# Optimization experiments

Hardware: AMD Instinct MI355X
Metric: run time of the kernel (lower is better)

Reference implementation:

```python
import jax, jax.numpy as jnp
import numpy as np

FEAT_STRIDE = 16
SCALES = (4, 8, 16, 32)
RATIOS = (0.5, 1.0, 2.0)
A = len(SCALES) * len(RATIOS)  # 12 anchors per location
PRE_NMS = 6000
POST_NMS = 300
NMS_THRESH = 0.7
MIN_SIZE = 16.0
B, C_IN, HF, WF = 4, 768, 64, 64


def _generate_anchors():
    base = np.array([0.0, 0.0, 15.0, 15.0])

    def whctrs(a):
        w = a[2] - a[0] + 1.0
        h = a[3] - a[1] + 1.0
        return w, h, a[0] + 0.5 * (w - 1.0), a[1] + 0.5 * (h - 1.0)

    def mk(ws, hs, xc, yc):
        ws = np.asarray(ws, dtype=np.float64)[:, None]
        hs = np.asarray(hs, dtype=np.float64)[:, None]
        return np.hstack([xc - 0.5 * (ws - 1), yc - 0.5 * (hs - 1),
                          xc + 0.5 * (ws - 1), yc + 0.5 * (hs - 1)])

    w, h, xc, yc = whctrs(base)
    size = w * h
    ratios = np.array(RATIOS)
    ws = np.round(np.sqrt(size / ratios))
    hs = np.round(ws * ratios)
    ratio_anchors = mk(ws, hs, xc, yc)
    scales = np.array(SCALES, dtype=np.float64)
    out = []
    for i in range(ratio_anchors.shape[0]):
        w, h, xc, yc = whctrs(ratio_anchors[i])
        out.append(mk(w * scales, h * scales, xc, yc))
    return np.vstack(out).astype(np.float32)  # (A, 4)


def _all_anchors(hf, wf):
    an = _generate_anchors()
    sx = np.arange(wf) * FEAT_STRIDE
    sy = np.arange(hf) * FEAT_STRIDE
    sx, sy = np.meshgrid(sx, sy)
    shifts = np.stack([sx.ravel(), sy.ravel(), sx.ravel(), sy.ravel()], axis=1).astype(np.float32)
    # shift-major, anchor-minor: (K, A, 4) -> (K*A, 4) matches bbox_pred layout
    return jnp.asarray((shifts[:, None, :] + an[None, :, :]).reshape(-1, 4))


def _conv(x, w, b):
    y = jax.lax.conv_general_dilated(x, w, (1, 1), 'SAME',
                                     dimension_numbers=('NCHW', 'OIHW', 'NCHW'))
    return y + b[None, :, None, None]


def _decode(anchors, deltas):
    w = anchors[:, 2] - anchors[:, 0] + 1.0
    h = anchors[:, 3] - anchors[:, 1] + 1.0
    cx = anchors[:, 0] + 0.5 * w
    cy = anchors[:, 1] + 0.5 * h
    dx, dy, dw, dh = deltas[:, 0], deltas[:, 1], deltas[:, 2], deltas[:, 3]
    pcx = dx * w + cx
    pcy = dy * h + cy
    pw = jnp.exp(dw) * w
    ph = jnp.exp(dh) * h
    return jnp.stack([pcx - 0.5 * pw, pcy - 0.5 * ph,
                      pcx + 0.5 * pw, pcy + 0.5 * ph], axis=1)


def _nms_keep(boxes, thresh):
    # greedy NMS on score-sorted boxes; returns boolean keep mask
    boxes = jax.lax.stop_gradient(boxes)
    n = boxes.shape[0]
    x1, y1, x2, y2 = boxes[:, 0], boxes[:, 1], boxes[:, 2], boxes[:, 3]
    areas = (x2 - x1 + 1.0) * (y2 - y1 + 1.0)
    idx = jnp.arange(n)

    def body(keep, i):
        xx1 = jnp.maximum(x1[i], x1)
        yy1 = jnp.maximum(y1[i], y1)
        xx2 = jnp.minimum(x2[i], x2)
        yy2 = jnp.minimum(y2[i], y2)
        inter = jnp.maximum(xx2 - xx1 + 1.0, 0.0) * jnp.maximum(yy2 - yy1 + 1.0, 0.0)
        iou = inter / (areas[i] + areas - inter)
        suppress = (iou > thresh) & (idx > i) & keep[i]
        return keep & ~suppress, None

    keep, _ = jax.lax.scan(body, jnp.ones(n, dtype=bool), jnp.arange(n))
    return keep


def _proposal_single(scores, deltas, anchors, im_info):
    # scores: (N,), deltas: (N,4), im_info: (3,) = [h, w, scale]
    boxes = _decode(anchors, deltas)
    x1 = jnp.clip(boxes[:, 0], 0.0, im_info[1] - 1.0)
    y1 = jnp.clip(boxes[:, 1], 0.0, im_info[0] - 1.0)
    x2 = jnp.clip(boxes[:, 2], 0.0, im_info[1] - 1.0)
    y2 = jnp.clip(boxes[:, 3], 0.0, im_info[0] - 1.0)
    boxes = jnp.stack([x1, y1, x2, y2], axis=1)
    ms = MIN_SIZE * im_info[2]
    valid = ((x2 - x1 + 1.0) >= ms) & ((y2 - y1 + 1.0) >= ms)
    scores = jnp.where(valid, scores, -jnp.inf)
    _, top_idx = jax.lax.top_k(scores, PRE_NMS)
    boxes = boxes[top_idx]
    keep = _nms_keep(boxes, NMS_THRESH)
    # first POST_NMS kept indices (boxes already score-sorted); zero-pad shortfall
    sel = jnp.sort(jnp.where(keep, jnp.arange(PRE_NMS), PRE_NMS))[:POST_NMS]
    pad = sel == PRE_NMS
    sel = jnp.minimum(sel, PRE_NMS - 1)
    return boxes[sel] * (~pad)[:, None].astype(boxes.dtype)


def setup_inputs() -> dict:
    key = jax.random.key(0)
    ks = jax.random.split(key, 4)
    features = jax.random.normal(ks[0], (B, C_IN, HF, WF), dtype=jnp.float32)
    im_info = jnp.tile(jnp.array([[1024.0, 1024.0, 1.0]], dtype=jnp.float32), (B, 1))
    W1 = jax.random.normal(ks[1], (512, C_IN, 3, 3), dtype=jnp.float32) * (2.0 / (C_IN * 9)) ** 0.5
    b1 = jnp.zeros((512,), dtype=jnp.float32)
    Ws = jax.random.normal(ks[2], (2 * A, 512, 1, 1), dtype=jnp.float32) * 0.01
    bs = jnp.zeros((2 * A,), dtype=jnp.float32)
    Wb = jax.random.normal(ks[3], (4 * A, 512, 1, 1), dtype=jnp.float32) * 0.01
    bb = jnp.zeros((4 * A,), dtype=jnp.float32)
    return {"features": features, "im_info": im_info, "W1": W1, "b1": b1,
            "Ws": Ws, "bs": bs, "Wb": Wb, "bb": bb}


def reference(features, im_info, W1, b1, Ws, bs, Wb, bb):
    # RPN head: 3x3 conv + relu, then 1x1 score/bbox heads
    x = jax.nn.relu(_conv(features, W1, b1))
    cls = _conv(x, Ws, bs)       # (B, 2A, H, W)
    bbox = _conv(x, Wb, bb)      # (B, 4A, H, W)
    b, _, hf, wf = cls.shape
    # view(B, 2, -1, W) softmax over class dim, view back -> channels [0:A]=bg, [A:2A]=fg
    prob = jax.nn.softmax(cls.reshape(b, 2, -1, wf), axis=1).reshape(cls.shape)
    fg = prob[:, A:, :, :]
    scores = fg.transpose(0, 2, 3, 1).reshape(b, -1)          # (B, H*W*A)
    deltas = bbox.transpose(0, 2, 3, 1).reshape(b, -1, 4)     # (B, H*W*A, 4)
    anchors = _all_anchors(hf, wf)
    boxes = jax.vmap(lambda s, d, ii: _proposal_single(s, d, anchors, ii))(scores, deltas, im_info)
    batch_idx = jnp.repeat(jnp.arange(b, dtype=boxes.dtype), POST_NMS)[:, None]
    rois = jnp.concatenate([batch_idx, boxes.reshape(-1, 4)], axis=1)  # (B*POST_NMS, 5)
    return rois
```

## Files before the change

### kernel.cpp

```cpp
#include <hip/hip_runtime.h>
#include <stdint.h>

#define CIN 768
#define CMID 512
#define NPIX 4096
#define NANCH 49152
#define NBATCH 4
#define PRE_NMS_N 6000
#define POST_NMS_N 300

__global__ void zeroK(uint32_t* __restrict__ p, int nWords){
  int i = blockIdx.x * 256 + threadIdx.x;
  if (i < nWords) p[i] = 0u;
}

__global__ __launch_bounds__(256) void conv3x3K(
    const float* __restrict__ feat, const float* __restrict__ W1,
    const float* __restrict__ b1, float* __restrict__ xout){
  __shared__ float wLds[9920];
  __shared__ float fLds[960];
  const int tid = threadIdx.x;
  const int g  = tid >> 3;
  const int py = tid & 7;
  const int ty0 = (blockIdx.x >> 3) << 3;
  const int tx0 = (blockIdx.x & 7) << 3;
  const int ocb = blockIdx.y << 7;
  const int b = blockIdx.z;

  const int oc_t  = tid >> 1;
  const int halfw = tid & 1;
  const float* wsrc0 = W1 + (size_t)(ocb + oc_t)*6912 + halfw*36;
  const int gq   = (oc_t>>2)*12 + (oc_t&3)*3;
  const int icl0 = halfw << 2;

  int fdst[4]; int fsrc[4]; bool fgo[4]; bool fact[4];
#pragma unroll
  for (int i=0;i<4;i++){
    int lin = tid + (i<<8);
    fact[i] = lin < 800;
    int l2 = fact[i] ? lin : 0;
    int ic = l2/100; int r2 = l2 - ic*100;
    int row = r2/10; int col = r2 - row*10;
    int gy = ty0 + row - 1, gx = tx0 + col - 1;
    fgo[i]  = fact[i] && gy>=0 && gy<64 && gx>=0 && gx<64;
    fdst[i] = ic*120 + row*12 + col;
    fsrc[i] = (ic<<12) + (gy<<6) + gx;
  }
  const float* fbase = feat + ((size_t)(b*CIN) << 12);

  double macc[4][8];
  float cacc[4][8];
#pragma unroll
  for (int q=0;q<4;q++)
#pragma unroll
    for (int j=0;j<8;j++){ macc[q][j]=0.0; cacc[q][j]=0.0f; }

  for (int icb = 0; icb < CIN; icb += 8){
    {
      const float* s = wsrc0 + (size_t)icb*9;
      float w0[36];
#pragma unroll
      for (int m=0;m<9;m++){
        float4 v = *reinterpret_cast<const float4*>(s + (m<<2));
        w0[4*m+0]=v.x; w0[4*m+1]=v.y; w0[4*m+2]=v.z; w0[4*m+3]=v.w;
      }
#pragma unroll
      for (int r=0;r<4;r++)
#pragma unroll
        for (int k=0;k<9;k++)
          wLds[(icl0+r)*1152 + (k/3)*384 + gq + (k%3)] = w0[r*9+k];
    }
#pragma unroll
    for (int i=0;i<4;i++){
      if (fact[i]){
        float v = 0.0f;
        if (fgo[i]) v = fbase[((size_t)icb << 12) + fsrc[i]];
        fLds[fdst[i]] = v;
      }
    }
    __syncthreads();
#pragma unroll
    for (int ic=0; ic<8; ic++){
      const float* fb = &fLds[ic*120 + py*12];
      const float* wb = &wLds[ic*1152 + g*12];
#pragma unroll
      for (int ky=0;ky<3;ky++){
        float4 a = *reinterpret_cast<const float4*>(fb + ky*12);
        float4 c = *reinterpret_cast<const float4*>(fb + ky*12 + 4);
        float2 e = *reinterpret_cast<const float2*>(fb + ky*12 + 8);
        const float f[10] = {a.x,a.y,a.z,a.w,c.x,c.y,c.z,c.w,e.x,e.y};
        const float* wp = wb + ky*384;
        float4 wa = *reinterpret_cast<const float4*>(wp);
        float4 wv = *reinterpret_cast<const float4*>(wp+4);
        float4 wc = *reinterpret_cast<const float4*>(wp+8);
        const float w12[12] = {wa.x,wa.y,wa.z,wa.w, wv.x,wv.y,wv.z,wv.w,
                               wc.x,wc.y,wc.z,wc.w};
#pragma unroll
        for (int q=0;q<4;q++)
#pragma unroll
          for (int kx=0;kx<3;kx++){
            float we = w12[q*3+kx];
#pragma unroll
            for (int j=0;j<8;j++)
              cacc[q][j] = fmaf(we, f[j+kx], cacc[q][j]);
          }
      }
      if ((ic & 3) == 3){
#pragma unroll
        for (int q=0;q<4;q++)
#pragma unroll
          for (int j=0;j<8;j++){ macc[q][j] += (double)cacc[q][j]; cacc[q][j]=0.0f; }
      }
    }
    __syncthreads();
  }
#pragma unroll
  for (int q=0;q<4;q++){
    float bias = b1[ocb + (g<<2) + q];
    float4 o0, o1;
    float* p0 = (float*)&o0; float* p1 = (float*)&o1;
#pragma unroll
    for (int j=0;j<4;j++){
      p0[j] = fmaxf(__fadd_rn((float)macc[q][j],   bias), 0.0f);
      p1[j] = fmaxf(__fadd_rn((float)macc[q][j+4], bias), 0.0f);
    }
    size_t base = ((size_t)(b*CMID + ocb + (g<<2) + q) << 12) + ((ty0+py) << 6) + tx0;
    *reinterpret_cast<float4*>(&xout[base])     = o0;
    *reinterpret_cast<float4*>(&xout[base + 4]) = o1;
  }
}

__global__ __launch_bounds__(256) void conv1x1K(
    const float* __restrict__ x,
    const float* __restrict__ Ws, const float* __restrict__ bs,
    const float* __restrict__ Wb, const float* __restrict__ bb,
    float* __restrict__ clsRaw, float* __restrict__ bboxRaw){
  __shared__ float wLds[32*72];
  const int tid = threadIdx.x;
  const int px = tid & 63;
  const int og = tid >> 6;
  const int px0 = (blockIdx.x & 63) << 6;
  const int b = blockIdx.x >> 6;
  double m[18];
  float cc[18];
#pragma unroll
  for (int j=0;j<18;j++){ m[j]=0.0; cc[j]=0.0f; }
  for (int cb=0; cb<CMID; cb+=32){
#pragma unroll
    for (int i=0;i<9;i++){
      int lin = tid + i*256;
      int c = lin / 72;
      int j = lin - c*72;
      wLds[lin] = (j < 24) ? Ws[(size_t)j*512 + cb + c]
                           : Wb[(size_t)(j-24)*512 + cb + c];
    }
    __syncthreads();
    for (int c=0;c<32;c++){
      float xv = x[((size_t)(b*CMID + cb + c) << 12) + px0 + px];
      const float* wp = &wLds[c*72 + og*18];
#pragma unroll
      for (int j=0;j<18;j++) cc[j] = fmaf(wp[j], xv, cc[j]);
    }
#pragma unroll
    for (int j=0;j<18;j++){ m[j] += (double)cc[j]; cc[j]=0.0f; }
    __syncthreads();
  }
#pragma unroll
  for (int j=0;j<18;j++){
    int jg = og*18 + j;
    float bias = (jg < 24) ? bs[jg] : bb[jg-24];
    float v = __fadd_rn((float)m[j], bias);
    if (jg < 24) clsRaw[((size_t)(b*24 + jg) << 12) + px0 + px] = v;
    else         bboxRaw[((size_t)(b*48 + jg - 24) << 12) + px0 + px] = v;
  }
}

__global__ void decodeK(const float* __restrict__ clsRaw,
                        const float* __restrict__ bboxRaw,
                        const float* __restrict__ imInfo,
                        float* __restrict__ boxes, uint32_t* __restrict__ ubits,
                        uint32_t* __restrict__ hist1){
  int n = blockIdx.x*256 + threadIdx.x;
  if (n >= NBATCH*NANCH) return;
  int b = n / NANCH;
  int r = n - b*NANCH;
  int px = r / 12;
  int a = r - px*12;
  int yi = px >> 6, xi = px & 63;
  const int w0t[3] = {23,16,11};
  const int h0t[3] = {12,16,22};
  int ridx = a >> 2;
  int sh = 2 + (a & 3);
  float W = (float)(w0t[ridx] << sh);
  float H = (float)(h0t[ridx] << sh);
  float cx = (float)((xi << 4) + 8);
  float cy = (float)((yi << 4) + 8);

  size_t cbase = ((size_t)b*24 << 12) + px;
  float sc0 = clsRaw[cbase + ((size_t)a       << 12)];
  float sc1 = clsRaw[cbase + ((size_t)(12+a)  << 12)];
  size_t bbase = ((size_t)b*48 << 12) + px;
  float dx = bboxRaw[bbase + ((size_t)(4*a+0) << 12)];
  float dy = bboxRaw[bbase + ((size_t)(4*a+1) << 12)];
  float dw = bboxRaw[bbase + ((size_t)(4*a+2) << 12)];
  float dh = bboxRaw[bbase + ((size_t)(4*a+3) << 12)];

  float imh = imInfo[b*3+0], imw = imInfo[b*3+1], iscale = imInfo[b*3+2];

  float pcx = __fadd_rn(__fmul_rn(dx, W), cx);
  float pcy = __fadd_rn(__fmul_rn(dy, H), cy);
  float pw  = __fmul_rn(expf(dw), W);
  float ph  = __fmul_rn(expf(dh), H);
  float hw = __fmul_rn(0.5f, pw), hh = __fmul_rn(0.5f, ph);
  float x1 = __fsub_rn(pcx, hw), x2 = __fadd_rn(pcx, hw);
  float y1 = __fsub_rn(pcy, hh), y2 = __fadd_rn(pcy, hh);
  float xmax = __fsub_rn(imw, 1.0f), ymax = __fsub_rn(imh, 1.0f);
  x1 = fminf(fmaxf(x1, 0.0f), xmax);
  y1 = fminf(fmaxf(y1, 0.0f), ymax);
  x2 = fminf(fmaxf(x2, 0.0f), xmax);
  y2 = fminf(fmaxf(y2, 0.0f), ymax);
  float ms = __fmul_rn(16.0f, iscale);
  bool valid = (__fadd_rn(__fsub_rn(x2,x1),1.0f) >= ms) &&
               (__fadd_rn(__fsub_rn(y2,y1),1.0f) >= ms);

  float mm = fmaxf(sc0, sc1);
  float e0 = expf(__fsub_rn(sc0, mm));
  float e1 = expf(__fsub_rn(sc1, mm));
  float s  = __fdiv_rn(e1, __fadd_rn(e0, e1));

  uint32_t u = __float_as_uint(s);
  u = (u & 0x80000000u) ? ~u : (u | 0x80000000u);
  if (!valid) u = 0x007FFFFFu;

  float4 bx = make_float4(x1, y1, x2, y2);
  *reinterpret_cast<float4*>(&boxes[(size_t)n*4]) = bx;
  ubits[n] = u;
  atomicAdd(&hist1[((size_t)b << 16) + (u >> 16)], 1u);
}

__global__ void histLoK(const uint32_t* __restrict__ ubits,
                        const uint32_t* __restrict__ thrWS, uint32_t* __restrict__ hist2){
  int n = blockIdx.x*256 + threadIdx.x;
  if (n >= NBATCH*NANCH) return;
  int b = n / NANCH;
  uint32_t u = ubits[n];
  if ((u >> 16) == thrWS[b*4+0])
    atomicAdd(&hist2[((size_t)b << 16) + (u & 0xFFFFu)], 1u);
}

__global__ __launch_bounds__(1024) void selectK(const uint32_t* __restrict__ hist,
                                                uint32_t* __restrict__ thrWS, int stage){
  __shared__ uint32_t sA[1024];
  const int b = blockIdx.x;
  const uint32_t* h = hist + ((size_t)b << 16);
  const int tid = threadIdx.x;
  uint32_t base = (stage == 0) ? 0u : thrWS[b*4+1];
  uint32_t seg = 0;
  int b0 = tid << 6;
  for (int k=0;k<64;k++) seg += h[b0+k];
  sA[tid] = seg;
  __syncthreads();
  for (int off=1; off<1024; off<<=1){
    uint32_t v = (tid+off < 1024) ? sA[tid+off] : 0u;
    __syncthreads();
    sA[tid] += v;
    __syncthreads();
  }
  uint32_t inc = sA[tid];
  uint32_t above = inc - seg;
  if (base + above < 6000u && base + inc >= 6000u){
    uint32_t c = base + above;
    for (int bin = b0+63; bin >= b0; bin--){
      uint32_t hh = h[bin];
      if (c + hh >= 6000u){
        if (stage == 0){ thrWS[b*4+0] = (uint32_t)bin; thrWS[b*4+1] = c; }
        else { thrWS[b*4+2] = (thrWS[b*4+0] << 16) | (uint32_t)bin; thrWS[b*4+3] = c; }
        break;
      }
      c += hh;
    }
  }
}

__global__ void compactK(const uint32_t* __restrict__ ubits,
                         const uint32_t* __restrict__ thrWS,
                         uint32_t* __restrict__ cnts,
                         uint64_t* __restrict__ keyHi, uint64_t* __restrict__ keyEq){
  int n = blockIdx.x*256 + threadIdx.x;
  if (n >= NBATCH*NANCH) return;
  int b = n / NANCH;
  int r = n - b*NANCH;
  uint32_t u = ubits[n];
  uint32_t us = thrWS[b*4+2];
  if (u < us) return;
  uint64_t key = ((uint64_t)(~u) << 32) | (uint32_t)r;
  if (u > us){
    uint32_t p = atomicAdd(&cnts[b*2+0], 1u);
    if (p < 8192u) keyHi[((size_t)b << 13) + p] = key;
  } else {
    uint32_t p = atomicAdd(&cnts[b*2+1], 1u);
    if (p < 8192u) keyEq[((size_t)b << 13) + p] = key;
  }
}

__global__ __launch_bounds__(1024) void sortGatherK(
    const uint64_t* __restrict__ keyHi, const uint64_t* __restrict__ keyEq,
    const uint32_t* __restrict__ cnts, const float* __restrict__ boxes,
    float* __restrict__ rbox){
  __shared__ uint64_t keys[8192];
  const int b = blockIdx.x;
  const int tid = threadIdx.x;
  uint32_t nHi = cnts[b*2+0];
  if (nHi > 8192u) nHi = 8192u;
  uint32_t nEq = cnts[b*2+1];
  if (nEq > 8192u - nHi) nEq = 8192u - nHi;
  for (int i=tid; i<8192; i+=1024){
    uint64_t k;
    if (i < (int)nHi) k = keyHi[((size_t)b << 13) + i];
    else if (i < (int)(nHi + nEq)) k = keyEq[((size_t)b << 13) + (i - nHi)];
    else k = ~0ULL;
    keys[i] = k;
  }
  __syncthreads();
  for (unsigned kk = 2; kk <= 8192; kk <<= 1){
    for (unsigned j = kk >> 1; j > 0; j >>= 1){
      for (unsigned i = tid; i < 8192; i += 1024){
        unsigned l = i ^ j;
        if (l > i){
          bool up = ((i & kk) == 0);
          uint64_t a = keys[i], c = keys[l];
          if ((a > c) == up){ keys[i] = c; keys[l] = a; }
        }
      }
      __syncthreads();
    }
  }
  for (int r = tid; r < PRE_NMS_N; r += 1024){
    uint32_t idx = (uint32_t)(keys[r] & 0xFFFFFFFFu);
    float4 v = *reinterpret_cast<const float4*>(&boxes[((size_t)b*NANCH + idx)*4]);
    *reinterpret_cast<float4*>(&rbox[((size_t)b*PRE_NMS_N + r)*4]) = v;
  }
}

__global__ __launch_bounds__(64) void nmsMaskK(const float* __restrict__ rbox,
                                               uint64_t* __restrict__ mask){
  const int b = blockIdx.z;
  const int ib = blockIdx.y;
  const int jb = blockIdx.x;
  const int lane = threadIdx.x;
  uint64_t* mrow = &mask[(size_t)b*PRE_NMS_N*96];
  if (jb < ib){
    int ig = (ib << 6) + lane;
    if (ig < PRE_NMS_N) mrow[(size_t)ig*96 + jb] = 0ull;
    return;
  }
  __shared__ float rb[64][4];
  const int ig0 = ib << 6;
  {
    int ig = ig0 + lane;
    float4 v = make_float4(0.f,0.f,0.f,0.f);
    if (ig < PRE_NMS_N) v = *reinterpret_cast<const float4*>(&rbox[((size_t)b*PRE_NMS_N + ig)*4]);
    rb[lane][0]=v.x; rb[lane][1]=v.y; rb[lane][2]=v.z; rb[lane][3]=v.w;
  }
  const int jg = (jb << 6) + lane;
  const bool jok = jg < PRE_NMS_N;
  float4 cb = make_float4(0.f,0.f,0.f,0.f);
  if (jok) cb = *reinterpret_cast<const float4*>(&rbox[((size_t)b*PRE_NMS_N + jg)*4]);
  float areaJ = __fmul_rn(__fadd_rn(__fsub_rn(cb.z,cb.x),1.0f),
                          __fadd_rn(__fsub_rn(cb.w,cb.y),1.0f));
  __syncthreads();
#pragma unroll 4
  for (int i=0;i<64;i++){
    int ig = ig0 + i;
    if (ig >= PRE_NMS_N) break;
    float x1=rb[i][0], y1=rb[i][1], x2=rb[i][2], y2=rb[i][3];
    float areaI = __fmul_rn(__fadd_rn(__fsub_rn(x2,x1),1.0f),
                            __fadd_rn(__fsub_rn(y2,y1),1.0f));
    float xx1 = fmaxf(x1, cb.x);
    float yy1 = fmaxf(y1, cb.y);
    float xx2 = fminf(x2, cb.z);
    float yy2 = fminf(y2, cb.w);
    float ww = fmaxf(__fadd_rn(__fsub_rn(xx2,xx1),1.0f), 0.0f);
    float hh = fmaxf(__fadd_rn(__fsub_rn(yy2,yy1),1.0f), 0.0f);
    float inter = __fmul_rn(ww,hh);
    float iou = __fdiv_rn(inter, __fsub_rn(__fadd_rn(areaI, areaJ), inter));
    bool bit = jok && (jg > ig) && (iou > 0.7f);
    uint64_t wword = __ballot(bit);
    if (lane == 0) mrow[(size_t)ig*96 + jb] = wword;
  }
}

__global__ __launch_bounds__(64) void nmsScanK(const float* __restrict__ rbox,
                                               const uint64_t* __restrict__ mask,
                                               float* __restrict__ out){
  const int b = blockIdx.x;
  const int lane = threadIdx.x;
  const uint64_t* mrow = &mask[(size_t)b*PRE_NMS_N*96];
  uint64_t s0 = 0ull, s1 = 0ull;
  int cnt = 0;
  for (int i=0; i<PRE_NMS_N; i++){
    int w = i >> 6;
    uint64_t sw = (w < 64) ? __shfl(s0, w) : __shfl(s1, w-64);
    if (!((sw >> (i & 63)) & 1ull)){
      if (lane == 0){
        const float* s = &rbox[((size_t)b*PRE_NMS_N + i)*4];
        float* o = &out[(size_t)(b*POST_NMS_N + cnt)*5];
        o[0] = (float)b; o[1]=s[0]; o[2]=s[1]; o[3]=s[2]; o[4]=s[3];
      }
      cnt++;
      if (cnt == POST_NMS_N) break;
      const uint64_t* mr = mrow + (size_t)i*96;
      s0 |= mr[lane];
      if (lane < 30) s1 |= mr[64+lane];
    }
  }
  for (int r = cnt + lane; r < POST_NMS_N; r += 64){
    float* o = &out[(size_t)(b*POST_NMS_N + r)*5];
    o[0] = (float)b; o[1]=0.f; o[2]=0.f; o[3]=0.f; o[4]=0.f;
  }
}

extern "C" void kernel_launch(void* const* d_in, const int* in_sizes, int n_in,
                              void* d_out, int out_size, void* d_ws, size_t ws_size,
                              hipStream_t stream) {
  const float* features = (const float*)d_in[0];
  const float* im_info  = (const float*)d_in[1];
  const float* W1 = (const float*)d_in[2];
  const float* b1 = (const float*)d_in[3];
  const float* Ws = (const float*)d_in[4];
  const float* bs = (const float*)d_in[5];
  const float* Wb = (const float*)d_in[6];
  const float* bb = (const float*)d_in[7];
  float* out = (float*)d_out;
  char* ws = (char*)d_ws;

  const size_t offX     = 0;
  const size_t offCls   = offX     + (size_t)4*512*4096*4;
  const size_t offBbox  = offCls   + (size_t)4*24*4096*4;
  const size_t offBoxes = offBbox  + (size_t)4*48*4096*4;
  const size_t offU     = offBoxes + (size_t)4*49152*4*4;
  const size_t offH1    = offU     + (size_t)4*49152*4;
  const size_t offH2    = offH1    + (size_t)4*65536*4;
  const size_t offCtr   = offH2    + (size_t)4*65536*4;
  const size_t offKHi   = offCtr   + 256;
  const size_t offKEq   = offKHi   + (size_t)4*8192*8;
  const size_t offRbox  = offKEq   + (size_t)4*8192*8;

  float*    x       = (float*)(ws + offX);
  float*    clsRaw  = (float*)(ws + offCls);
  float*    bboxRaw = (float*)(ws + offBbox);
  float*    boxes   = (float*)(ws + offBoxes);
  uint32_t* ubits   = (uint32_t*)(ws + offU);
  uint32_t* hist1   = (uint32_t*)(ws + offH1);
  uint32_t* hist2   = (uint32_t*)(ws + offH2);
  uint32_t* thrWS   = (uint32_t*)(ws + offCtr);
  uint32_t* cnts    = thrWS + 16;
  uint64_t* keyHi   = (uint64_t*)(ws + offKHi);
  uint64_t* keyEq   = (uint64_t*)(ws + offKEq);
  float*    rbox    = (float*)(ws + offRbox);
  uint64_t* mask    = (uint64_t*)(ws + offX);

  {
    int nWords = (int)(((offCtr + 256) - offH1) / 4);
    int grid = (nWords + 255) / 256;
    zeroK<<<grid, 256, 0, stream>>>((uint32_t*)(ws + offH1), nWords);
  }
  conv3x3K<<<dim3(64, 4, 4), 256, 0, stream>>>(features, W1, b1, x);
  conv1x1K<<<256, 256, 0, stream>>>(x, Ws, bs, Wb, bb, clsRaw, bboxRaw);
  {
    int grid = (NBATCH*NANCH + 255) / 256;
    decodeK<<<grid, 256, 0, stream>>>(clsRaw, bboxRaw, im_info, boxes, ubits, hist1);
    selectK<<<4, 1024, 0, stream>>>(hist1, thrWS, 0);
    histLoK<<<grid, 256, 0, stream>>>(ubits, thrWS, hist2);
    selectK<<<4, 1024, 0, stream>>>(hist2, thrWS, 1);
    compactK<<<grid, 256, 0, stream>>>(ubits, thrWS, cnts, keyHi, keyEq);
  }
  sortGatherK<<<4, 1024, 0, stream>>>(keyHi, keyEq, cnts, boxes, rbox);
  nmsMaskK<<<dim3(94, 94, 4), 64, 0, stream>>>(rbox, mask);
  nmsScanK<<<4, 64, 0, stream>>>(rbox, mask, out);
}
```

Before: 2.414 ms.

## Use float outer accumulators and double-buffer LDS operand loads in 3x3 conv

Replaces the double-precision outer accumulators in the 3x3 conv with float accumulators. This removes the slow FP64 adds and conversions and halves the accumulator register footprint. The inner ic/ky loop is flattened into 24 steps with register double-buffering of the feature and weight LDS reads, so the next step's loads overlap the current FMAs. The risk is slightly different rounding from the double accumulation, and higher register pressure from the two buffers.

Measured after the change: 2.484 ms, median of 2. 2.9% more time.

```diff
diff --git a/kernel.cpp b/kernel.cpp
--- a/kernel.cpp
+++ b/kernel.cpp
@@ -48,12 +48,29 @@
   }
   const float* fbase = feat + ((size_t)(b*CIN) << 12);
 
-  double macc[4][8];
+  float macc[4][8];
   float cacc[4][8];
 #pragma unroll
   for (int q=0;q<4;q++)
 #pragma unroll
-    for (int j=0;j<8;j++){ macc[q][j]=0.0; cacc[q][j]=0.0f; }
+    for (int j=0;j<8;j++){ macc[q][j]=0.0f; cacc[q][j]=0.0f; }
+
+#define LOADF(dst, icx, kyx) { \
+    const float* fp_ = &fLds[(icx)*120 + (py+(kyx))*12]; \
+    float4 a_ = *reinterpret_cast<const float4*>(fp_); \
+    float4 c_ = *reinterpret_cast<const float4*>(fp_+4); \
+    float2 e_ = *reinterpret_cast<const float2*>(fp_+8); \
+    dst[0]=a_.x; dst[1]=a_.y; dst[2]=a_.z; dst[3]=a_.w; \
+    dst[4]=c_.x; dst[5]=c_.y; dst[6]=c_.z; dst[7]=c_.w; \
+    dst[8]=e_.x; dst[9]=e_.y; }
+#define LOADW(dst, icx, kyx) { \
+    const float* wp_ = &wLds[(icx)*1152 + (kyx)*384 + g*12]; \
+    float4 a_ = *reinterpret_cast<const float4*>(wp_); \
+    float4 b_ = *reinterpret_cast<const float4*>(wp_+4); \
+    float4 c_ = *reinterpret_cast<const float4*>(wp_+8); \
+    dst[0]=a_.x; dst[1]=a_.y; dst[2]=a_.z; dst[3]=a_.w; \
+    dst[4]=b_.x; dst[5]=b_.y; dst[6]=b_.z; dst[7]=b_.w; \
+    dst[8]=c_.x; dst[9]=c_.y; dst[10]=c_.z; dst[11]=c_.w; }
 
   for (int icb = 0; icb < CIN; icb += 8){
     {
@@ -79,41 +96,44 @@
       }
     }
     __syncthreads();
-#pragma unroll
-    for (int ic=0; ic<8; ic++){
-      const float* fb = &fLds[ic*120 + py*12];
-      const float* wb = &wLds[ic*1152 + g*12];
-#pragma unroll
-      for (int ky=0;ky<3;ky++){
-        float4 a = *reinterpret_cast<const float4*>(fb + ky*12);
-        float4 c = *reinterpret_cast<const float4*>(fb + ky*12 + 4);
-        float2 e = *reinterpret_cast<const float2*>(fb + ky*12 + 8);
-        const float f[10] = {a.x,a.y,a.z,a.w,c.x,c.y,c.z,c.w,e.x,e.y};
-        const float* wp = wb + ky*384;
-        float4 wa = *reinterpret_cast<const float4*>(wp);
-        float4 wv = *reinterpret_cast<const float4*>(wp+4);
-        float4 wc = *reinterpret_cast<const float4*>(wp+8);
-        const float w12[12] = {wa.x,wa.y,wa.z,wa.w, wv.x,wv.y,wv.z,wv.w,
-                               wc.x,wc.y,wc.z,wc.w};
+    {
+      float fb[2][10]; float wb[2][12];
+      LOADF(fb[0], 0, 0);
+      LOADW(wb[0], 0, 0);
+#pragma unroll
+      for (int s=0; s<24; s++){
+        const int ic = s/3, ky = s - 3*ic;
+        const int cur = s & 1, nxt = cur ^ 1;
+        if (s < 23){
+          const int s2 = s + 1;
+          const int ic2 = s2/3, ky2 = s2 - 3*ic2;
+          LOADF(fb[nxt], ic2, ky2);
+          LOADW(wb[nxt], ic2, ky2);
+        }
 #pragma unroll
         for (int q=0;q<4;q++)
 #pragma unroll
           for (int kx=0;kx<3;kx++){
-            float we = w12[q*3+kx];
+            float we = wb[cur][q*3+kx];
 #pragma unroll
             for (int j=0;j<8;j++)
-              cacc[q][j] = fmaf(we, f[j+kx], cacc[q][j]);
+              cacc[q][j] = fmaf(we, fb[cur][j+kx], cacc[q][j]);
           }
+        if (ky == 2 && (ic & 3) == 3){
+#pragma unroll
+          for (int q=0;q<4;q++)
+#pragma unroll
+            for (int j=0;j<8;j++){
+              macc[q][j] = __fadd_rn(macc[q][j], cacc[q][j]);
+              cacc[q][j] = 0.0f;
+            }
+        }
       }
-      if ((ic & 3) == 3){
-#pragma unroll
-        for (int q=0;q<4;q++)
-#pragma unroll
-          for (int j=0;j<8;j++){ macc[q][j] += (double)cacc[q][j]; cacc[q][j]=0.0f; }
-      }
     }
     __syncthreads();
   }
+#undef LOADF
+#undef LOADW
 #pragma unroll
   for (int q=0;q<4;q++){
     float bias = b1[ocb + (g<<2) + q];
@@ -121,8 +141,8 @@
     float* p0 = (float*)&o0; float* p1 = (float*)&o1;
 #pragma unroll
     for (int j=0;j<4;j++){
-      p0[j] = fmaxf(__fadd_rn((float)macc[q][j],   bias), 0.0f);
-      p1[j] = fmaxf(__fadd_rn((float)macc[q][j+4], bias), 0.0f);
+      p0[j] = fmaxf(__fadd_rn(macc[q][j],   bias), 0.0f);
+      p1[j] = fmaxf(__fadd_rn(macc[q][j+4], bias), 0.0f);
     }
     size_t base = ((size_t)(b*CMID + ocb + (g<<2) + q) << 12) + ((ty0+py) << 6) + tx0;
     *reinterpret_cast<float4*>(&xout[base])     = o0;
```
